# Optimization experiments

Measured on AMD Instinct MI355X. Metric: run time of the kernel, lower is better.

## Reference

```python
import jax, jax.numpy as jnp
import numpy as np

N = 100000   # nodes
E = 1600000  # edges
F = 128      # n_feat
HID = 64     # n_hid
L = 4        # n_layer
C = 40       # n_class
TEMP = 0.1   # summarize temperature


def setup_inputs() -> dict:
    key = jax.random.key(0)
    ks = jax.random.split(key, 10)
    x = jax.random.normal(ks[0], (N, F), dtype=jnp.float32)
    edge_index = jax.random.randint(ks[1], (2, E), 0, N, dtype=jnp.int64)
    s_in = 1.0 / np.sqrt(F)
    s_h = 1.0 / np.sqrt(HID)
    W0 = jax.random.normal(ks[2], (F, HID), dtype=jnp.float32) * s_in
    b0 = jnp.zeros((HID,), dtype=jnp.float32)
    Ws = jax.random.normal(ks[3], (L - 1, HID, HID), dtype=jnp.float32) * s_h
    bs = jnp.zeros((L - 1, HID), dtype=jnp.float32)
    Wq = jax.random.normal(ks[4], (HID, HID), dtype=jnp.float32) * s_h
    Wk = jax.random.normal(ks[5], (HID, HID), dtype=jnp.float32) * s_h
    Wout = jax.random.normal(ks[6], (HID, C), dtype=jnp.float32) * s_h
    bout = jnp.zeros((C,), dtype=jnp.float32)
    return {"x": x, "edge_index": edge_index, "W0": W0, "b0": b0,
            "Ws": Ws, "bs": bs, "Wq": Wq, "Wk": Wk, "Wout": Wout, "bout": bout}


def reference(x, edge_index, W0, b0, Ws, bs, Wq, Wk, Wout, bout):
    # --- GCN normalization with self-loops (symmetric D^-1/2 (A+I) D^-1/2) ---
    loop = jnp.arange(N, dtype=edge_index.dtype)
    src = jnp.concatenate([edge_index[0], loop])  # [E+N]
    dst = jnp.concatenate([edge_index[1], loop])
    deg = jax.ops.segment_sum(jnp.ones_like(dst, dtype=x.dtype), dst, num_segments=N)
    dinv = jnp.where(deg > 0, jax.lax.rsqrt(deg), 0.0)
    enorm = dinv[src] * dinv[dst]  # [E+N]

    def propagate(h):
        # gather -> scale -> scatter-add (sparse matvec)
        msg = h[src] * enorm[:, None]
        return jax.ops.segment_sum(msg, dst, num_segments=N)

    # --- twin-branch stacked GCN convs (x_ starts as detached copy; eval mode => no dropout) ---
    h, h_ = x, x
    hs, hs_ = [], []
    for l in range(L):
        W = W0 if l == 0 else Ws[l - 1]
        b = b0 if l == 0 else bs[l - 1]
        h = jax.nn.relu(propagate(h @ W) + b)
        h_ = jax.nn.relu(propagate(h_ @ W) + b)
        hs.append(h)
        hs_.append(h_)

    Hm = jnp.stack(hs)    # [L, N, HID]
    Hm_ = jnp.stack(hs_)  # [L, N, HID]

    # --- Summarize: per-node attention over layer scales; query from twin branch ---
    q = jnp.einsum('lnd,de->lne', Hm_, Wq)
    k = jnp.einsum('lnd,de->lne', Hm, Wk)
    scores = jnp.sum(q * k, axis=-1) / TEMP      # [L, N]
    att = jax.nn.softmax(scores, axis=0)         # softmax over layers
    hsum = jnp.einsum('ln,lnd->nd', att, Hm)     # [N, HID]

    return hsum @ Wout + bout                    # [N, C]
```

## Files before the change

kernel.cpp:

```cpp
#include <hip/hip_runtime.h>
#include <hip/hip_bf16.h>
#include <math.h>

#define NN 100000
#define EE 1600000
#define FF 128
#define HH 64
#define CC 40

constexpr int SCAN_B = 1024;
constexpr int NB = (NN + SCAN_B - 1) / SCAN_B;

typedef unsigned long long u64;
typedef float f32x4 __attribute__((ext_vector_type(4)));

constexpr int RN = NN / 8;
constexpr int BCAP = 220000;
constexpr int NE_BLK = 2000;
constexpr int ABLK = EE / NE_BLK;
constexpr int GBLK = 128;
constexpr int SELFB2 = (RN + GBLK - 1) / GBLK;

__global__ void k_init(int* __restrict__ deg, int* __restrict__ bcnt) {
    int i = blockIdx.x * 256 + threadIdx.x;
    if (i < NN) deg[i] = 1;
    if (i < 8) bcnt[i] = 0;
}

__global__ __launch_bounds__(256) void k_bucket(const int* __restrict__ ei, int* __restrict__ bcnt,
                                                u64* __restrict__ bpr) {
    __shared__ int lcnt[8], lbase[8], loff[8];
    const int t = threadIdx.x;
    if (t < 8) { lcnt[t] = 0; loff[t] = 0; }
    __syncthreads();
    const int e0 = blockIdx.x * NE_BLK;
    int es[8], ed[8];
    int kmax = 0;
#pragma unroll
    for (int k = 0; k < 8; ++k) {
        int e = e0 + t + k * 256;
        if (t + k * 256 < NE_BLK) {
            es[k] = ei[e];
            ed[k] = ei[EE + e];
            atomicAdd(&lcnt[ed[k] / RN], 1);
            kmax = k + 1;
        }
    }
    __syncthreads();
    if (t < 8) lbase[t] = atomicAdd(&bcnt[t], lcnt[t]);
    __syncthreads();
#pragma unroll
    for (int k = 0; k < 8; ++k) {
        if (k < kmax) {
            int b = ed[k] / RN;
            int pos = lbase[b] + atomicAdd(&loff[b], 1);
            if (pos < BCAP) {
                bpr[(size_t)b * BCAP + pos] = (u64)(unsigned)es[k] | ((u64)(unsigned)ed[k] << 32);
            }
        }
    }
}

__global__ void k_count2(const u64* __restrict__ bpr, const int* __restrict__ bcnt,
                         int* __restrict__ deg) {
    const int g = blockIdx.x & 7;
    const int j = blockIdx.x >> 3;
    const int cnt = bcnt[g];
    const u64* __restrict__ pp = bpr + (size_t)g * BCAP;
    for (int i = j * 256 + threadIdx.x; i < cnt; i += GBLK * 256) {
        atomicAdd(&deg[(int)(pp[i] >> 32)], 1);
    }
}

__global__ void k_dinv(const int* __restrict__ deg, float* __restrict__ dinv) {
    int i = blockIdx.x * 256 + threadIdx.x;
    if (i < NN) dinv[i] = rsqrtf((float)deg[i]);
}

__global__ void k_scanA(const int* __restrict__ deg, int* __restrict__ excl, int* __restrict__ bsum) {
    __shared__ int s[SCAN_B];
    int t = threadIdx.x;
    int g = blockIdx.x * SCAN_B + t;
    int v = (g < NN) ? deg[g] : 0;
    s[t] = v;
    __syncthreads();
    for (int o = 1; o < SCAN_B; o <<= 1) {
        int u = (t >= o) ? s[t - o] : 0;
        __syncthreads();
        s[t] += u;
        __syncthreads();
    }
    if (g < NN) excl[g] = s[t] - v;
    if (t == SCAN_B - 1) bsum[blockIdx.x] = s[t];
}

__global__ void k_scanB(int* __restrict__ bsum) {
    __shared__ int s[128];
    int t = threadIdx.x;
    int v = (t < NB) ? bsum[t] : 0;
    s[t] = v;
    __syncthreads();
    for (int o = 1; o < 128; o <<= 1) {
        int u = (t >= o) ? s[t - o] : 0;
        __syncthreads();
        s[t] += u;
        __syncthreads();
    }
    if (t < NB) bsum[t] = s[t] - v;
}

__global__ void k_scanC(int* __restrict__ rp, const int* __restrict__ bsum, int* __restrict__ cursor) {
    int t = threadIdx.x;
    int g = blockIdx.x * SCAN_B + t;
    if (g < NN) {
        int v = rp[g] + bsum[blockIdx.x];
        rp[g] = v;
        cursor[g] = v;
    }
    if (g == 0) rp[NN] = EE + NN;
}

__global__ void k_fill2(const u64* __restrict__ bpr, const int* __restrict__ bcnt,
                        int* __restrict__ cursor, int* __restrict__ cs) {
    const int g = blockIdx.x & 7;
    const int j = blockIdx.x >> 3;
    const int cnt = bcnt[g];
    const u64* __restrict__ pp = bpr + (size_t)g * BCAP;
    for (int i = j * 256 + threadIdx.x; i < cnt; i += GBLK * 256) {
        u64 u = pp[i];
        int d = (int)(u >> 32);
        int p = atomicAdd(&cursor[d], 1);
        cs[p] = (int)(unsigned)u;
    }
    const int lo = g * RN;
    int n = lo + j * SELFB2 + threadIdx.x;
    if (threadIdx.x < SELFB2 && n < lo + RN) {
        int p = atomicAdd(&cursor[n], 1);
        cs[p] = n;
    }
}

template <int K>
__global__ __launch_bounds__(256) void k_gemm(const float* __restrict__ A, const float* __restrict__ W,
                                              const float* __restrict__ dinv, float* __restrict__ Z,
                                              int nrows) {
    constexpr int S = 68;
    __shared__ float wl[64 * 64];
    __shared__ float hl[64 * S];
    const int t = threadIdx.x;
    const int r0 = blockIdx.x * 64;
    const int rg = t >> 4, cg = t & 15;
    float acc[4][4] = {};

    for (int kb = 0; kb < K; kb += 64) {
        {
            const float4* Wv = (const float4*)(W + kb * 64);
            for (int i = t; i < 1024; i += 256) ((float4*)wl)[i] = Wv[i];
        }
        for (int i = t; i < 1024; i += 256) {
            int row = i >> 4, d4 = i & 15;
            float4 v = {0.f, 0.f, 0.f, 0.f};
            if (r0 + row < nrows) v = *(const float4*)(A + (size_t)(r0 + row) * K + kb + d4 * 4);
            *(float4*)(hl + row * S + d4 * 4) = v;
        }
        __syncthreads();
#pragma unroll 8
        for (int d = 0; d < 64; ++d) {
            float4 w4 = *(const float4*)(wl + d * 64 + cg * 4);
#pragma unroll
            for (int i = 0; i < 4; i++) {
                float h = hl[(rg * 4 + i) * S + d];
                acc[i][0] = fmaf(h, w4.x, acc[i][0]);
                acc[i][1] = fmaf(h, w4.y, acc[i][1]);
                acc[i][2] = fmaf(h, w4.z, acc[i][2]);
                acc[i][3] = fmaf(h, w4.w, acc[i][3]);
            }
        }
        __syncthreads();
    }
#pragma unroll
    for (int i = 0; i < 4; i++) {
        int row = r0 + rg * 4 + i;
        if (row < nrows) {
            float dv = dinv[row];
            float4 o = {acc[i][0] * dv, acc[i][1] * dv, acc[i][2] * dv, acc[i][3] * dv};
            *(float4*)(Z + (size_t)row * 64 + cg * 4) = o;
        }
    }
}

__global__ __launch_bounds__(256) void k_prepM(const float* __restrict__ Wq, const float* __restrict__ Wk,
                                               float* __restrict__ M) {
    __shared__ float wk[64 * 65];
    __shared__ float wq[4 * 64];
    const int t = threadIdx.x;
    for (int i = t; i < 1024; i += 256) {
        int r = i >> 4, c4 = i & 15;
        float4 v = ((const float4*)Wk)[i];
        wk[r * 65 + c4 * 4 + 0] = v.x;
        wk[r * 65 + c4 * 4 + 1] = v.y;
        wk[r * 65 + c4 * 4 + 2] = v.z;
        wk[r * 65 + c4 * 4 + 3] = v.w;
    }
    const int rbase = blockIdx.x * 4;
    wq[t] = Wq[rbase * 64 + t];
    __syncthreads();
    const int rr = t >> 6;
    const int c = t & 63;
    float acc = 0.f;
#pragma unroll 8
    for (int e = 0; e < 64; ++e) acc = fmaf(wq[rr * 64 + e], wk[c * 65 + e], acc);
    M[(rbase + rr) * 64 + c] = acc;
}

__global__ __launch_bounds__(256) void k_score(const float* __restrict__ Hm, const float* __restrict__ M,
                                               float* __restrict__ scores) {
    constexpr int S = 68;
    __shared__ float wl[4096];
    __shared__ float hl[64 * S];
    const int t = threadIdx.x;
    const int r0 = blockIdx.x * 64;
    for (int i = t; i < 1024; i += 256) ((float4*)wl)[i] = ((const float4*)M)[i];
    for (int i = t; i < 1024; i += 256) {
        int row = i >> 4, d4 = i & 15;
        *(float4*)(hl + row * S + d4 * 4) = *(const float4*)(Hm + (size_t)(r0 + row) * 64 + d4 * 4);
    }
    __syncthreads();
    const int rg = t >> 4, cg = t & 15;
    float u[4][4] = {};
#pragma unroll 8
    for (int d = 0; d < 64; ++d) {
        float4 m4 = *(const float4*)(wl + d * 64 + cg * 4);
#pragma unroll
        for (int i = 0; i < 4; i++) {
            float h = hl[(rg * 4 + i) * S + d];
            u[i][0] = fmaf(h, m4.x, u[i][0]);
            u[i][1] = fmaf(h, m4.y, u[i][1]);
            u[i][2] = fmaf(h, m4.z, u[i][2]);
            u[i][3] = fmaf(h, m4.w, u[i][3]);
        }
    }
#pragma unroll
    for (int i = 0; i < 4; i++) {
        const float* hrow = hl + (rg * 4 + i) * S + cg * 4;
        float p = u[i][0] * hrow[0] + u[i][1] * hrow[1] + u[i][2] * hrow[2] + u[i][3] * hrow[3];
        p += __shfl_xor(p, 1);
        p += __shfl_xor(p, 2);
        p += __shfl_xor(p, 4);
        p += __shfl_xor(p, 8);
        if (cg == 0) scores[r0 + rg * 4 + i] = p;
    }
}

__global__ __launch_bounds__(256) void k_prop(const float* __restrict__ z, const int* __restrict__ rp,
                                              const int* __restrict__ cs, const float* __restrict__ dinv,
                                              const float* __restrict__ bias, float* __restrict__ out) {
    const int lane = threadIdx.x & 63;
    const int g = lane >> 4;
    const int l4 = lane & 15;
    const int n = blockIdx.x * 16 + (threadIdx.x >> 6) * 4 + g;
    const int beg = rp[n], end = rp[n + 1];
    float4 a0 = {0, 0, 0, 0}, a1 = {0, 0, 0, 0}, a2 = {0, 0, 0, 0}, a3 = {0, 0, 0, 0};
    int i = beg;
    for (; i + 8 <= end; i += 8) {
        int c0 = __builtin_nontemporal_load(cs + i);
        int c1 = __builtin_nontemporal_load(cs + i + 1);
        int c2 = __builtin_nontemporal_load(cs + i + 2);
        int c3 = __builtin_nontemporal_load(cs + i + 3);
        int c4 = __builtin_nontemporal_load(cs + i + 4);
        int c5 = __builtin_nontemporal_load(cs + i + 5);
        int c6 = __builtin_nontemporal_load(cs + i + 6);
        int c7 = __builtin_nontemporal_load(cs + i + 7);
        float4 z0 = *(const float4*)(z + (size_t)(unsigned)c0 * 64 + l4 * 4);
        float4 z1 = *(const float4*)(z + (size_t)(unsigned)c1 * 64 + l4 * 4);
        float4 z2 = *(const float4*)(z + (size_t)(unsigned)c2 * 64 + l4 * 4);
        float4 z3 = *(const float4*)(z + (size_t)(unsigned)c3 * 64 + l4 * 4);
        float4 z4 = *(const float4*)(z + (size_t)(unsigned)c4 * 64 + l4 * 4);
        float4 z5 = *(const float4*)(z + (size_t)(unsigned)c5 * 64 + l4 * 4);
        float4 z6 = *(const float4*)(z + (size_t)(unsigned)c6 * 64 + l4 * 4);
        float4 z7 = *(const float4*)(z + (size_t)(unsigned)c7 * 64 + l4 * 4);
        a0.x += z0.x; a0.y += z0.y; a0.z += z0.z; a0.w += z0.w;
        a1.x += z1.x; a1.y += z1.y; a1.z += z1.z; a1.w += z1.w;
        a2.x += z2.x; a2.y += z2.y; a2.z += z2.z; a2.w += z2.w;
        a3.x += z3.x; a3.y += z3.y; a3.z += z3.z; a3.w += z3.w;
        a0.x += z4.x; a0.y += z4.y; a0.z += z4.z; a0.w += z4.w;
        a1.x += z5.x; a1.y += z5.y; a1.z += z5.z; a1.w += z5.w;
        a2.x += z6.x; a2.y += z6.y; a2.z += z6.z; a2.w += z6.w;
        a3.x += z7.x; a3.y += z7.y; a3.z += z7.z; a3.w += z7.w;
    }
    for (; i + 4 <= end; i += 4) {
        int c0 = __builtin_nontemporal_load(cs + i);
        int c1 = __builtin_nontemporal_load(cs + i + 1);
        int c2 = __builtin_nontemporal_load(cs + i + 2);
        int c3 = __builtin_nontemporal_load(cs + i + 3);
        float4 z0 = *(const float4*)(z + (size_t)(unsigned)c0 * 64 + l4 * 4);
        float4 z1 = *(const float4*)(z + (size_t)(unsigned)c1 * 64 + l4 * 4);
        float4 z2 = *(const float4*)(z + (size_t)(unsigned)c2 * 64 + l4 * 4);
        float4 z3 = *(const float4*)(z + (size_t)(unsigned)c3 * 64 + l4 * 4);
        a0.x += z0.x; a0.y += z0.y; a0.z += z0.z; a0.w += z0.w;
        a1.x += z1.x; a1.y += z1.y; a1.z += z1.z; a1.w += z1.w;
        a2.x += z2.x; a2.y += z2.y; a2.z += z2.z; a2.w += z2.w;
        a3.x += z3.x; a3.y += z3.y; a3.z += z3.z; a3.w += z3.w;
    }
    for (; i < end; ++i) {
        int c = __builtin_nontemporal_load(cs + i);
        float4 zr = *(const float4*)(z + (size_t)(unsigned)c * 64 + l4 * 4);
        a0.x += zr.x; a0.y += zr.y; a0.z += zr.z; a0.w += zr.w;
    }
    const float dn = dinv[n];
    const float4 b4 = *(const float4*)(bias + l4 * 4);
    float4 r;
    r.x = fmaf(dn, (a0.x + a1.x) + (a2.x + a3.x), b4.x);
    r.y = fmaf(dn, (a0.y + a1.y) + (a2.y + a3.y), b4.y);
    r.z = fmaf(dn, (a0.z + a1.z) + (a2.z + a3.z), b4.z);
    r.w = fmaf(dn, (a0.w + a1.w) + (a2.w + a3.w), b4.w);
    r.x = r.x > 0.f ? r.x : 0.f;
    r.y = r.y > 0.f ? r.y : 0.f;
    r.z = r.z > 0.f ? r.z : 0.f;
    r.w = r.w > 0.f ? r.w : 0.f;
    __builtin_nontemporal_store(*(const f32x4*)&r, (f32x4*)(out + (size_t)n * 64 + l4 * 4));
}

__global__ __launch_bounds__(256) void k_sum(const float* __restrict__ Hm, const float* __restrict__ scores,
                                             const float* __restrict__ Wout, const float* __restrict__ bout,
                                             float* __restrict__ out) {
    __shared__ float wo[64 * CC];
    __shared__ float hs[64][68];
    __shared__ float wl4[4][64];
    const int t = threadIdx.x;
    const int r0 = blockIdx.x * 64;
    for (int i = t; i < (64 * CC) / 4; i += 256) ((float4*)wo)[i] = ((const float4*)Wout)[i];
    if (t < 64) {
        int n = r0 + t;
        float s0 = 0.f, s1 = 0.f, s2 = 0.f, s3 = 0.f;
        if (n < NN) {
            s0 = scores[0 * NN + n] * 10.f;
            s1 = scores[1 * NN + n] * 10.f;
            s2 = scores[2 * NN + n] * 10.f;
            s3 = scores[3 * NN + n] * 10.f;
        }
        float m = fmaxf(fmaxf(s0, s1), fmaxf(s2, s3));
        float e0 = __expf(s0 - m), e1 = __expf(s1 - m), e2 = __expf(s2 - m), e3 = __expf(s3 - m);
        float inv = 1.f / (e0 + e1 + e2 + e3);
        wl4[0][t] = e0 * inv;
        wl4[1][t] = e1 * inv;
        wl4[2][t] = e2 * inv;
        wl4[3][t] = e3 * inv;
    }
    __syncthreads();
    for (int i = t; i < 1024; i += 256) {
        int row = i >> 4, d4 = i & 15;
        int n = r0 + row;
        float4 acc = {0.f, 0.f, 0.f, 0.f};
        if (n < NN) {
#pragma unroll
            for (int l = 0; l < 4; ++l) {
                float w = wl4[l][row];
                float4 h = *(const float4*)(Hm + ((size_t)l * NN + n) * 64 + d4 * 4);
                acc.x = fmaf(w, h.x, acc.x);
                acc.y = fmaf(w, h.y, acc.y);
                acc.z = fmaf(w, h.z, acc.z);
                acc.w = fmaf(w, h.w, acc.w);
            }
        }
        *(float4*)(&hs[row][d4 * 4]) = acc;
    }
    __syncthreads();
    const int row = t >> 2, cg = t & 3;
    float2 acc2[5] = {};
    for (int d = 0; d < 64; ++d) {
        float a = hs[row][d];
        const float2* wrow = (const float2*)(wo + d * CC + cg * 10);
#pragma unroll
        for (int j = 0; j < 5; ++j) {
            float2 w = wrow[j];
            acc2[j].x = fmaf(a, w.x, acc2[j].x);
            acc2[j].y = fmaf(a, w.y, acc2[j].y);
        }
    }
    int n = r0 + row;
    if (n < NN) {
        float* op = out + (size_t)n * CC + cg * 10;
        const float* bp = bout + cg * 10;
#pragma unroll
        for (int j = 0; j < 5; ++j) {
            float2 b = *(const float2*)(bp + 2 * j);
            float2 o = {acc2[j].x + b.x, acc2[j].y + b.y};
            *(float2*)(op + 2 * j) = o;
        }
    }
}

extern "C" void kernel_launch(void* const* d_in, const int* in_sizes, int n_in,
                              void* d_out, int out_size, void* d_ws, size_t ws_size,
                              hipStream_t stream) {
    const float* x    = (const float*)d_in[0];
    const int*   ei   = (const int*)d_in[1];
    const float* W0   = (const float*)d_in[2];
    const float* b0   = (const float*)d_in[3];
    const float* Ws   = (const float*)d_in[4];
    const float* bs   = (const float*)d_in[5];
    const float* Wq   = (const float*)d_in[6];
    const float* Wk   = (const float*)d_in[7];
    const float* Wout = (const float*)d_in[8];
    const float* bout = (const float*)d_in[9];
    float* out = (float*)d_out;

    char* p = (char*)d_ws;
    auto carve = [&](size_t bytes) {
        void* r = (void*)p;
        p += (bytes + 255) & ~(size_t)255;
        return r;
    };
    int*   deg     = (int*)carve((size_t)NN * 4);
    float* dinv    = (float*)carve((size_t)NN * 4);
    int*   row_ptr = (int*)carve((size_t)(NN + 1) * 4);
    int*   cursor  = (int*)carve((size_t)NN * 4);
    int*   bsum    = (int*)carve(256 * 4);
    int*   bcnt    = (int*)carve(8 * 4);
    u64*   bpr     = (u64*)carve((size_t)8 * BCAP * 8);
    int*   cs      = (int*)carve((size_t)(EE + NN) * 4);
    float* M       = (float*)carve((size_t)HH * HH * 4);
    float* z       = (float*)carve((size_t)NN * HH * 4);
    float* Hm      = (float*)carve((size_t)4 * NN * HH * 4);
    float* scores  = (float*)carve((size_t)4 * NN * 4);
    (void)ws_size; (void)n_in; (void)in_sizes; (void)out_size;

    const int GB_N  = (NN + 255) / 256;
    const int GT    = (NN + 63) / 64;
    const int GSC   = (4 * NN) / 64;
    const int GP    = NN / 16;
    const int GS2   = (NN + 63) / 64;

    k_init<<<GB_N, 256, 0, stream>>>(deg, bcnt);
    k_bucket<<<ABLK, 256, 0, stream>>>(ei, bcnt, bpr);
    k_count2<<<GBLK * 8, 256, 0, stream>>>(bpr, bcnt, deg);
    k_dinv<<<GB_N, 256, 0, stream>>>(deg, dinv);
    k_scanA<<<NB, SCAN_B, 0, stream>>>(deg, row_ptr, bsum);
    k_scanB<<<1, 128, 0, stream>>>(bsum);
    k_scanC<<<NB, SCAN_B, 0, stream>>>(row_ptr, bsum, cursor);
    k_fill2<<<GBLK * 8, 256, 0, stream>>>(bpr, bcnt, cursor, cs);
    k_prepM<<<16, 256, 0, stream>>>(Wq, Wk, M);

    k_gemm<FF><<<GT, 256, 0, stream>>>(x, W0, dinv, z, NN);
    k_prop<<<GP, 256, 0, stream>>>(z, row_ptr, cs, dinv, b0, Hm);
    for (int l = 1; l < 4; ++l) {
        k_gemm<HH><<<GT, 256, 0, stream>>>(Hm + (size_t)(l - 1) * NN * HH,
                                           Ws + (size_t)(l - 1) * HH * HH, dinv, z, NN);
        k_prop<<<GP, 256, 0, stream>>>(z, row_ptr, cs, dinv, bs + (size_t)(l - 1) * HH,
                                       Hm + (size_t)l * NN * HH);
    }

    k_score<<<GSC, 256, 0, stream>>>(Hm, M, scores);
    k_sum<<<GS2, 256, 0, stream>>>(Hm, scores, Wout, bout, out);
}
```

Baseline: 695.6 us.

## Build CSR via fine-grained buckets with LDS histogram/fill and fuse score into summary kernel

Edges are partitioned into 125 buckets of 800 destination nodes, so degree counting and CSR column fill run per-bucket in shared memory. Each bucket's column segment is then written out contiguously, replacing scattered global atomics on per-node cursors. Separately, the attention score kernel is merged into the summarize/output kernel, which drops the scores buffer round trip and one launch. Risks include bucket overflow if a bucket exceeds the 13800-edge capacity, and a large per-block LDS footprint (about 58KB) in the fill kernel that limits occupancy.

```diff
diff --git a/kernel.cpp b/kernel.cpp
--- a/kernel.cpp
+++ b/kernel.cpp
@@ -14,62 +14,62 @@
 typedef unsigned long long u64;
 typedef float f32x4 __attribute__((ext_vector_type(4)));
 
-constexpr int RN = NN / 8;
-constexpr int BCAP = 220000;
-constexpr int NE_BLK = 2000;
+constexpr int NBUK = 125;
+constexpr int RNB = 800;
+constexpr int BCAP3 = 13800;
+constexpr int NE_BLK = 4000;
 constexpr int ABLK = EE / NE_BLK;
-constexpr int GBLK = 128;
-constexpr int SELFB2 = (RN + GBLK - 1) / GBLK;
-
-__global__ void k_init(int* __restrict__ deg, int* __restrict__ bcnt) {
-    int i = blockIdx.x * 256 + threadIdx.x;
-    if (i < NN) deg[i] = 1;
-    if (i < 8) bcnt[i] = 0;
+
+__global__ void k_init(int* __restrict__ bcnt) {
+    int i = threadIdx.x;
+    if (i < NBUK) bcnt[i] = 0;
 }
 
 __global__ __launch_bounds__(256) void k_bucket(const int* __restrict__ ei, int* __restrict__ bcnt,
                                                 u64* __restrict__ bpr) {
-    __shared__ int lcnt[8], lbase[8], loff[8];
+    __shared__ int lcnt[NBUK], lbase[NBUK], loff[NBUK];
     const int t = threadIdx.x;
-    if (t < 8) { lcnt[t] = 0; loff[t] = 0; }
+    for (int k = t; k < NBUK; k += 256) { lcnt[k] = 0; loff[k] = 0; }
     __syncthreads();
     const int e0 = blockIdx.x * NE_BLK;
-    int es[8], ed[8];
-    int kmax = 0;
-#pragma unroll
-    for (int k = 0; k < 8; ++k) {
-        int e = e0 + t + k * 256;
-        if (t + k * 256 < NE_BLK) {
-            es[k] = ei[e];
-            ed[k] = ei[EE + e];
-            atomicAdd(&lcnt[ed[k] / RN], 1);
-            kmax = k + 1;
-        }
-    }
-    __syncthreads();
-    if (t < 8) lbase[t] = atomicAdd(&bcnt[t], lcnt[t]);
-    __syncthreads();
-#pragma unroll
-    for (int k = 0; k < 8; ++k) {
-        if (k < kmax) {
-            int b = ed[k] / RN;
+    int es[16], ed[16];
+#pragma unroll
+    for (int k = 0; k < 16; ++k) {
+        int idx = t + k * 256;
+        if (idx < NE_BLK) {
+            es[k] = ei[e0 + idx];
+            ed[k] = ei[EE + e0 + idx];
+            atomicAdd(&lcnt[ed[k] / RNB], 1);
+        }
+    }
+    __syncthreads();
+    for (int k = t; k < NBUK; k += 256) lbase[k] = atomicAdd(&bcnt[k], lcnt[k]);
+    __syncthreads();
+#pragma unroll
+    for (int k = 0; k < 16; ++k) {
+        int idx = t + k * 256;
+        if (idx < NE_BLK) {
+            int b = ed[k] / RNB;
             int pos = lbase[b] + atomicAdd(&loff[b], 1);
-            if (pos < BCAP) {
-                bpr[(size_t)b * BCAP + pos] = (u64)(unsigned)es[k] | ((u64)(unsigned)ed[k] << 32);
+            if (pos < BCAP3) {
+                bpr[(size_t)b * BCAP3 + pos] = (u64)(unsigned)es[k] | ((u64)(unsigned)ed[k] << 32);
             }
         }
     }
 }
 
-__global__ void k_count2(const u64* __restrict__ bpr, const int* __restrict__ bcnt,
-                         int* __restrict__ deg) {
-    const int g = blockIdx.x & 7;
-    const int j = blockIdx.x >> 3;
-    const int cnt = bcnt[g];
-    const u64* __restrict__ pp = bpr + (size_t)g * BCAP;
-    for (int i = j * 256 + threadIdx.x; i < cnt; i += GBLK * 256) {
-        atomicAdd(&deg[(int)(pp[i] >> 32)], 1);
-    }
+__global__ __launch_bounds__(512) void k_count3(const u64* __restrict__ bpr, const int* __restrict__ bcnt,
+                                                int* __restrict__ deg) {
+    __shared__ int h[RNB];
+    const int t = threadIdx.x, b = blockIdx.x;
+    for (int k = t; k < RNB; k += 512) h[k] = 0;
+    __syncthreads();
+    const int cnt = min(bcnt[b], BCAP3);
+    const u64* __restrict__ pp = bpr + (size_t)b * BCAP3;
+    const int lo = b * RNB;
+    for (int i = t; i < cnt; i += 512) atomicAdd(&h[(int)(pp[i] >> 32) - lo], 1);
+    __syncthreads();
+    for (int k = t; k < RNB; k += 512) deg[lo + k] = h[k] + 1;
 }
 
 __global__ void k_dinv(const int* __restrict__ deg, float* __restrict__ dinv) {
@@ -109,35 +109,37 @@
     if (t < NB) bsum[t] = s[t] - v;
 }
 
-__global__ void k_scanC(int* __restrict__ rp, const int* __restrict__ bsum, int* __restrict__ cursor) {
+__global__ void k_scanC(int* __restrict__ rp, const int* __restrict__ bsum) {
     int t = threadIdx.x;
     int g = blockIdx.x * SCAN_B + t;
-    if (g < NN) {
-        int v = rp[g] + bsum[blockIdx.x];
-        rp[g] = v;
-        cursor[g] = v;
-    }
+    if (g < NN) rp[g] = rp[g] + bsum[blockIdx.x];
     if (g == 0) rp[NN] = EE + NN;
 }
 
-__global__ void k_fill2(const u64* __restrict__ bpr, const int* __restrict__ bcnt,
-                        int* __restrict__ cursor, int* __restrict__ cs) {
-    const int g = blockIdx.x & 7;
-    const int j = blockIdx.x >> 3;
-    const int cnt = bcnt[g];
-    const u64* __restrict__ pp = bpr + (size_t)g * BCAP;
-    for (int i = j * 256 + threadIdx.x; i < cnt; i += GBLK * 256) {
+__global__ __launch_bounds__(512) void k_fill3(const u64* __restrict__ bpr, const int* __restrict__ bcnt,
+                                               const int* __restrict__ rp, int* __restrict__ cs) {
+    __shared__ int lcur[RNB];
+    __shared__ int lbuf[RNB + BCAP3];
+    const int t = threadIdx.x, b = blockIdx.x;
+    const int lo = b * RNB;
+    const int rpl = rp[lo];
+    for (int k = t; k < RNB; k += 512) lcur[k] = rp[lo + k] - rpl;
+    __syncthreads();
+    const int cnt = min(bcnt[b], BCAP3);
+    const u64* __restrict__ pp = bpr + (size_t)b * BCAP3;
+    for (int i = t; i < cnt; i += 512) {
         u64 u = pp[i];
-        int d = (int)(u >> 32);
-        int p = atomicAdd(&cursor[d], 1);
-        cs[p] = (int)(unsigned)u;
-    }
-    const int lo = g * RN;
-    int n = lo + j * SELFB2 + threadIdx.x;
-    if (threadIdx.x < SELFB2 && n < lo + RN) {
-        int p = atomicAdd(&cursor[n], 1);
-        cs[p] = n;
-    }
+        int pos = atomicAdd(&lcur[(int)(u >> 32) - lo], 1);
+        lbuf[pos] = (int)(unsigned)u;
+    }
+    __syncthreads();
+    for (int k = t; k < RNB; k += 512) {
+        int pos = atomicAdd(&lcur[k], 1);
+        lbuf[pos] = lo + k;
+    }
+    __syncthreads();
+    const int total = rp[lo + RNB] - rpl;
+    for (int i = t; i < total; i += 512) __builtin_nontemporal_store(lbuf[i], cs + rpl + i);
 }
 
 template <int K>
@@ -211,45 +213,6 @@
 #pragma unroll 8
     for (int e = 0; e < 64; ++e) acc = fmaf(wq[rr * 64 + e], wk[c * 65 + e], acc);
     M[(rbase + rr) * 64 + c] = acc;
-}
-
-__global__ __launch_bounds__(256) void k_score(const float* __restrict__ Hm, const float* __restrict__ M,
-                                               float* __restrict__ scores) {
-    constexpr int S = 68;
-    __shared__ float wl[4096];
-    __shared__ float hl[64 * S];
-    const int t = threadIdx.x;
-    const int r0 = blockIdx.x * 64;
-    for (int i = t; i < 1024; i += 256) ((float4*)wl)[i] = ((const float4*)M)[i];
-    for (int i = t; i < 1024; i += 256) {
-        int row = i >> 4, d4 = i & 15;
-        *(float4*)(hl + row * S + d4 * 4) = *(const float4*)(Hm + (size_t)(r0 + row) * 64 + d4 * 4);
-    }
-    __syncthreads();
-    const int rg = t >> 4, cg = t & 15;
-    float u[4][4] = {};
-#pragma unroll 8
-    for (int d = 0; d < 64; ++d) {
-        float4 m4 = *(const float4*)(wl + d * 64 + cg * 4);
-#pragma unroll
-        for (int i = 0; i < 4; i++) {
-            float h = hl[(rg * 4 + i) * S + d];
-            u[i][0] = fmaf(h, m4.x, u[i][0]);
-            u[i][1] = fmaf(h, m4.y, u[i][1]);
-            u[i][2] = fmaf(h, m4.z, u[i][2]);
-            u[i][3] = fmaf(h, m4.w, u[i][3]);
-        }
-    }
-#pragma unroll
-    for (int i = 0; i < 4; i++) {
-        const float* hrow = hl + (rg * 4 + i) * S + cg * 4;
-        float p = u[i][0] * hrow[0] + u[i][1] * hrow[1] + u[i][2] * hrow[2] + u[i][3] * hrow[3];
-        p += __shfl_xor(p, 1);
-        p += __shfl_xor(p, 2);
-        p += __shfl_xor(p, 4);
-        p += __shfl_xor(p, 8);
-        if (cg == 0) scores[r0 + rg * 4 + i] = p;
-    }
 }
 
 __global__ __launch_bounds__(256) void k_prop(const float* __restrict__ z, const int* __restrict__ rp,
@@ -321,24 +284,56 @@
     __builtin_nontemporal_store(*(const f32x4*)&r, (f32x4*)(out + (size_t)n * 64 + l4 * 4));
 }
 
-__global__ __launch_bounds__(256) void k_sum(const float* __restrict__ Hm, const float* __restrict__ scores,
-                                             const float* __restrict__ Wout, const float* __restrict__ bout,
-                                             float* __restrict__ out) {
+__global__ __launch_bounds__(256) void k_scoresum(const float* __restrict__ Hm, const float* __restrict__ Mm,
+                                                  const float* __restrict__ Wout, const float* __restrict__ bout,
+                                                  float* __restrict__ out) {
+    __shared__ float wl[4096];
+    __shared__ float hl[64 * 68];
     __shared__ float wo[64 * CC];
-    __shared__ float hs[64][68];
+    __shared__ float sc[4][64];
     __shared__ float wl4[4][64];
     const int t = threadIdx.x;
     const int r0 = blockIdx.x * 64;
+    for (int i = t; i < 1024; i += 256) ((float4*)wl)[i] = ((const float4*)Mm)[i];
     for (int i = t; i < (64 * CC) / 4; i += 256) ((float4*)wo)[i] = ((const float4*)Wout)[i];
+    const int rg = t >> 4, cg = t & 15;
+    for (int l = 0; l < 4; ++l) {
+        __syncthreads();
+        for (int i = t; i < 1024; i += 256) {
+            int row = i >> 4, d4 = i & 15;
+            int n = r0 + row;
+            float4 v = {0.f, 0.f, 0.f, 0.f};
+            if (n < NN) v = *(const float4*)(Hm + ((size_t)l * NN + n) * 64 + d4 * 4);
+            *(float4*)(hl + row * 68 + d4 * 4) = v;
+        }
+        __syncthreads();
+        float u[4][4] = {};
+#pragma unroll 8
+        for (int d = 0; d < 64; ++d) {
+            float4 m4 = *(const float4*)(wl + d * 64 + cg * 4);
+#pragma unroll
+            for (int i = 0; i < 4; i++) {
+                float h = hl[(rg * 4 + i) * 68 + d];
+                u[i][0] = fmaf(h, m4.x, u[i][0]);
+                u[i][1] = fmaf(h, m4.y, u[i][1]);
+                u[i][2] = fmaf(h, m4.z, u[i][2]);
+                u[i][3] = fmaf(h, m4.w, u[i][3]);
+            }
+        }
+#pragma unroll
+        for (int i = 0; i < 4; i++) {
+            const float* hrow = hl + (rg * 4 + i) * 68 + cg * 4;
+            float p = u[i][0] * hrow[0] + u[i][1] * hrow[1] + u[i][2] * hrow[2] + u[i][3] * hrow[3];
+            p += __shfl_xor(p, 1);
+            p += __shfl_xor(p, 2);
+            p += __shfl_xor(p, 4);
+            p += __shfl_xor(p, 8);
+            if (cg == 0) sc[l][rg * 4 + i] = p;
+        }
+    }
+    __syncthreads();
     if (t < 64) {
-        int n = r0 + t;
-        float s0 = 0.f, s1 = 0.f, s2 = 0.f, s3 = 0.f;
-        if (n < NN) {
-            s0 = scores[0 * NN + n] * 10.f;
-            s1 = scores[1 * NN + n] * 10.f;
-            s2 = scores[2 * NN + n] * 10.f;
-            s3 = scores[3 * NN + n] * 10.f;
-        }
+        float s0 = sc[0][t] * 10.f, s1 = sc[1][t] * 10.f, s2 = sc[2][t] * 10.f, s3 = sc[3][t] * 10.f;
         float m = fmaxf(fmaxf(s0, s1), fmaxf(s2, s3));
         float e0 = __expf(s0 - m), e1 = __expf(s1 - m), e2 = __expf(s2 - m), e3 = __expf(s3 - m);
         float inv = 1.f / (e0 + e1 + e2 + e3);
@@ -363,14 +358,14 @@
                 acc.w = fmaf(w, h.w, acc.w);
             }
         }
-        *(float4*)(&hs[row][d4 * 4]) = acc;
-    }
-    __syncthreads();
-    const int row = t >> 2, cg = t & 3;
+        *(float4*)(hl + row * 68 + d4 * 4) = acc;
+    }
+    __syncthreads();
+    const int row2 = t >> 2, cg2 = t & 3;
     float2 acc2[5] = {};
     for (int d = 0; d < 64; ++d) {
-        float a = hs[row][d];
-        const float2* wrow = (const float2*)(wo + d * CC + cg * 10);
+        float a = hl[row2 * 68 + d];
+        const float2* wrow = (const float2*)(wo + d * CC + cg2 * 10);
 #pragma unroll
         for (int j = 0; j < 5; ++j) {
             float2 w = wrow[j];
@@ -378,10 +373,10 @@
             acc2[j].y = fmaf(a, w.y, acc2[j].y);
         }
     }
-    int n = r0 + row;
+    int n = r0 + row2;
     if (n < NN) {
-        float* op = out + (size_t)n * CC + cg * 10;
-        const float* bp = bout + cg * 10;
+        float* op = out + (size_t)n * CC + cg2 * 10;
+        const float* bp = bout + cg2 * 10;
 #pragma unroll
         for (int j = 0; j < 5; ++j) {
             float2 b = *(const float2*)(bp + 2 * j);
@@ -415,31 +410,28 @@
     int*   deg     = (int*)carve((size_t)NN * 4);
     float* dinv    = (float*)carve((size_t)NN * 4);
     int*   row_ptr = (int*)carve((size_t)(NN + 1) * 4);
-    int*   cursor  = (int*)carve((size_t)NN * 4);
     int*   bsum    = (int*)carve(256 * 4);
-    int*   bcnt    = (int*)carve(8 * 4);
-    u64*   bpr     = (u64*)carve((size_t)8 * BCAP * 8);
+    int*   bcnt    = (int*)carve(NBUK * 4);
+    u64*   bpr     = (u64*)carve((size_t)NBUK * BCAP3 * 8);
     int*   cs      = (int*)carve((size_t)(EE + NN) * 4);
     float* M       = (float*)carve((size_t)HH * HH * 4);
     float* z       = (float*)carve((size_t)NN * HH * 4);
     float* Hm      = (float*)carve((size_t)4 * NN * HH * 4);
-    float* scores  = (float*)carve((size_t)4 * NN * 4);
     (void)ws_size; (void)n_in; (void)in_sizes; (void)out_size;
 
-    const int GB_N  = (NN + 255) / 256;
-    const int GT    = (NN + 63) / 64;
-    const int GSC   = (4 * NN) / 64;
-    const int GP    = NN / 16;
-    const int GS2   = (NN + 63) / 64;
-
-    k_init<<<GB_N, 256, 0, stream>>>(deg, bcnt);
+    const int GB_N = (NN + 255) / 256;
+    const int GT   = (NN + 63) / 64;
+    const int GP   = NN / 16;
+    const int GSS  = (NN + 63) / 64;
+
+    k_init<<<1, 128, 0, stream>>>(bcnt);
     k_bucket<<<ABLK, 256, 0, stream>>>(ei, bcnt, bpr);
-    k_count2<<<GBLK * 8, 256, 0, stream>>>(bpr, bcnt, deg);
+    k_count3<<<NBUK, 512, 0, stream>>>(bpr, bcnt, deg);
     k_dinv<<<GB_N, 256, 0, stream>>>(deg, dinv);
     k_scanA<<<NB, SCAN_B, 0, stream>>>(deg, row_ptr, bsum);
     k_scanB<<<1, 128, 0, stream>>>(bsum);
-    k_scanC<<<NB, SCAN_B, 0, stream>>>(row_ptr, bsum, cursor);
-    k_fill2<<<GBLK * 8, 256, 0, stream>>>(bpr, bcnt, cursor, cs);
+    k_scanC<<<NB, SCAN_B, 0, stream>>>(row_ptr, bsum);
+    k_fill3<<<NBUK, 512, 0, stream>>>(bpr, bcnt, row_ptr, cs);
     k_prepM<<<16, 256, 0, stream>>>(Wq, Wk, M);
 
     k_gemm<FF><<<GT, 256, 0, stream>>>(x, W0, dinv, z, NN);
@@ -451,6 +443,5 @@
                                        Hm + (size_t)l * NN * HH);
     }
 
-    k_score<<<GSC, 256, 0, stream>>>(Hm, M, scores);
-    k_sum<<<GS2, 256, 0, stream>>>(Hm, scores, Wout, bout, out);
-}
+    k_scoresum<<<GSS, 256, 0, stream>>>(Hm, M, Wout, bout, out);
+}
```

Result: faster. 594.0 us (-14.6%).
